# Kernel tuning notes

Hardware: AMD Instinct MI355X
Metric: run time of the kernel (lower is better)

The kernel has to match this reference:

```python
import jax, jax.numpy as jnp
import numpy as np

BATCH, T, H, N = 16, 4096, 512, 512  # batch, seq_len, d_model, d_hidden
R_MAX, R_MIN, MAX_PHASE = 1.0, 0.0, 6.28


def setup_inputs() -> dict:
    key = jax.random.key(0)
    ks = jax.random.split(key, 8)
    u_k = jax.random.normal(ks[0], (BATCH, T, H), jnp.float32)
    x0_real = jnp.zeros((BATCH, N), jnp.float32)
    x0_imag = jnp.zeros((BATCH, N), jnp.float32)
    # LRU eigenvalue parameterization (Orvieto et al. 2023)
    u1 = jax.random.uniform(ks[1], (N,), jnp.float32)
    u2 = jax.random.uniform(ks[2], (N,), jnp.float32)
    nu_log = jnp.log(-0.5 * jnp.log(u1 * (R_MAX**2 - R_MIN**2) + R_MIN**2))
    theta_log = jnp.log(MAX_PHASE * u2)
    B_re = jax.random.normal(ks[3], (N, H), jnp.float32) / np.sqrt(2.0 * H)
    B_im = jax.random.normal(ks[4], (N, H), jnp.float32) / np.sqrt(2.0 * H)
    C_re = jax.random.normal(ks[5], (H, N), jnp.float32) / np.sqrt(N)
    C_im = jax.random.normal(ks[6], (H, N), jnp.float32) / np.sqrt(N)
    D = jax.random.normal(ks[7], (H,), jnp.float32)
    return dict(x0_real=x0_real, x0_imag=x0_imag, u_k=u_k, nu_log=nu_log,
                theta_log=theta_log, B_re=B_re, B_im=B_im, C_re=C_re,
                C_im=C_im, D=D)


def reference(x0_real, x0_imag, u_k, nu_log, theta_log, B_re, B_im, C_re, C_im, D):
    # diagonal complex eigenvalues lambda in the unit disk
    lam = jnp.exp(-jnp.exp(nu_log) + 1j * jnp.exp(theta_log))          # [N] complex64
    gamma = jnp.sqrt(1.0 - jnp.abs(lam) ** 2).astype(jnp.float32)       # [N]
    Bmat = (B_re + 1j * B_im) * gamma[:, None]                          # [N,H]
    # input projection: Bu[b,t,n] = sum_h Bmat[n,h] * u[b,t,h]
    Bu = jnp.einsum('bth,nh->btn', u_k.astype(jnp.complex64), Bmat)     # [B,T,N]
    # fold initial state into first step: x_1 = lam*x_0 + Bu_1
    x0 = x0_real + 1j * x0_imag                                         # [B,N]
    Bu = Bu.at[:, 0].add(lam[None, :] * x0)
    a = jnp.broadcast_to(lam, Bu.shape)                                 # [B,T,N]

    def combine(e1, e2):
        a1, b1 = e1
        a2, b2 = e2
        return a1 * a2, a2 * b1 + b2

    # parallel associative scan of x_k = lam*x_{k-1} + Bu_k
    _, xs = jax.lax.associative_scan(combine, (a, Bu), axis=1)          # [B,T,N]
    C = C_re + 1j * C_im                                                # [H,N]
    outs = jnp.einsum('btn,hn->bth', xs, C).real + D * u_k              # [B,T,H]
    return xs[:, -1], outs
```

## Files before the change

### kernel.cpp

```cpp
#include <hip/hip_runtime.h>

#define BATCH 16
#define TSEQ  4096
#define HDIM  512
#define NDIM  512
#define NCHUNK 64
#define LCHUNK 64

using f32x4  = __attribute__((ext_vector_type(4))) float;
using bf16x8 = __attribute__((ext_vector_type(8))) short;

typedef const __attribute__((address_space(1))) void GV;
typedef __attribute__((address_space(3))) void LV;

__device__ __forceinline__ void gload16(const void* g, void* l) {
  __builtin_amdgcn_global_load_lds((GV*)g, (LV*)l, 16, 0, 0);
}
__device__ __forceinline__ unsigned short f2bf(float f) {
  unsigned u = __float_as_uint(f);
  return (unsigned short)((u + 0x7fffu + ((u >> 16) & 1u)) >> 16);
}
__device__ __forceinline__ float bf2f(unsigned short s) {
  return __uint_as_float(((unsigned)s) << 16);
}

__global__ void prep_params(const float* __restrict__ nu_log,
                            const float* __restrict__ theta_log,
                            float* lam_re, float* lam_im, float* gam,
                            float* lamL_re, float* lamL_im) {
  int n = threadIdx.x;
  float en = expf(nu_log[n]);
  float th = expf(theta_log[n]);
  float r  = expf(-en);
  lam_re[n] = r * cosf(th);
  lam_im[n] = r * sinf(th);
  float r2 = expf(-2.f * en);
  gam[n] = sqrtf(fmaxf(1.f - r2, 0.f));
  float rL  = expf(-(float)LCHUNK * en);
  float thL = (float)LCHUNK * th;
  lamL_re[n] = rL * cosf(thL);
  lamL_im[n] = rL * sinf(thL);
}

__global__ void prep_bcat(const float* __restrict__ B_re, const float* __restrict__ B_im,
                          const float* __restrict__ gam, unsigned short* __restrict__ Bcat) {
  int idx = blockIdx.x * 256 + threadIdx.x;
  int h   = idx & (HDIM - 1);
  int row = idx >> 9;
  int n   = row >> 1;
  float g = gam[n];
  float v = (row & 1) ? B_im[n * HDIM + h] : B_re[n * HDIM + h];
  Bcat[idx] = f2bf(g * v);
}

__global__ void prep_ccat(const float* __restrict__ C_re, const float* __restrict__ C_im,
                          unsigned short* __restrict__ Ccat) {
  int idx = blockIdx.x * 256 + threadIdx.x;
  int col = idx & (2 * NDIM - 1);
  int h   = idx >> 10;
  int n   = col >> 1;
  float v = (col & 1) ? -C_im[h * NDIM + n] : C_re[h * NDIM + n];
  Ccat[idx] = f2bf(v);
}

__global__ void conv_u(const float4* __restrict__ u, ushort4* __restrict__ ub, int n4) {
  int idx = blockIdx.x * 256 + threadIdx.x;
  if (idx >= n4) return;
  float4 v = u[idx];
  ushort4 o;
  o.x = f2bf(v.x); o.y = f2bf(v.y); o.z = f2bf(v.z); o.w = f2bf(v.w);
  ub[idx] = o;
}

template <int K, bool OUTBF>
__global__ __launch_bounds__(256)
void gemm97(const unsigned short* __restrict__ A,
            const unsigned short* __restrict__ Bm,
            void* __restrict__ Co, int Ncol, int Nd,
            const unsigned short* __restrict__ ub,
            const float* __restrict__ Dv) {
  __shared__ char lds[65536];
  const int tid  = threadIdx.x;
  const int wave = tid >> 6, lane = tid & 63;
  const int wr = (wave >> 1) * 64, wc = (wave & 1) * 64;

  int nwg = gridDim.x;
  int bid = blockIdx.x;
  int wg  = (bid & 7) * (nwg >> 3) + (bid >> 3);
  int bn = wg % Ncol, bm = wg / Ncol;
  const long rowBase = (long)bm * 128;
  const long colBase = (long)bn * 128;

  const int colE = 8 * ((tid & 7) ^ ((tid >> 3) & 7));
  const unsigned short* srcA[4];
  const unsigned short* srcB[4];
#pragma unroll
  for (int r = 0; r < 4; r++) {
    srcA[r] = A  + (rowBase + r * 32 + (tid >> 3)) * (long)K + colE;
    srcB[r] = Bm + (colBase + r * 32 + (tid >> 3)) * (long)K + colE;
  }

  f32x4 acc[4][4];
#pragma unroll
  for (int i = 0; i < 4; i++)
#pragma unroll
    for (int j = 0; j < 4; j++) acc[i][j] = (f32x4){0.f, 0.f, 0.f, 0.f};

  const int rsub = lane & 15;
  const int sx   = (lane & 7) << 4;
  const int ke   = (lane >> 4) << 4;

  for (int kt = 0; kt < K; kt += 64) {
    __syncthreads();
#pragma unroll
    for (int r = 0; r < 4; r++) {
      gload16(srcA[r] + kt, &lds[r * 4096 + tid * 16]);
      gload16(srcB[r] + kt, &lds[32768 + r * 4096 + tid * 16]);
    }
    __syncthreads();
#pragma unroll
    for (int kk = 0; kk < 64; kk += 32) {
      bf16x8 af[4], bf[4];
#pragma unroll
      for (int i = 0; i < 4; i++) {
        int off = (((wr + i * 16 + rsub) << 7) + kk * 2 + ke) ^ sx;
        af[i] = *(const bf16x8*)&lds[off];
      }
#pragma unroll
      for (int j = 0; j < 4; j++) {
        int off = 32768 + ((((wc + j * 16 + rsub) << 7) + kk * 2 + ke) ^ sx);
        bf[j] = *(const bf16x8*)&lds[off];
      }
#pragma unroll
      for (int i = 0; i < 4; i++)
#pragma unroll
        for (int j = 0; j < 4; j++)
          acc[i][j] = __builtin_amdgcn_mfma_f32_16x16x32_bf16(af[i], bf[j], acc[i][j], 0, 0, 0);
    }
  }

  const int cc = lane & 15, r4 = (lane >> 4) * 4;
#pragma unroll
  for (int i = 0; i < 4; i++) {
#pragma unroll
    for (int j = 0; j < 4; j++) {
      long col = colBase + wc + j * 16 + cc;
#pragma unroll
      for (int r = 0; r < 4; r++) {
        long row = rowBase + wr + i * 16 + r4 + r;
        if (OUTBF) {
          ((unsigned short*)Co)[row * (long)Nd + col] = f2bf(acc[i][j][r]);
        } else {
          float d = Dv[col];
          ((float*)Co)[row * (long)Nd + col] =
              acc[i][j][r] + d * bf2f(ub[row * (long)Nd + col]);
        }
      }
    }
  }
}

__global__ void scan_carry(const unsigned* __restrict__ Bu,
                           const float* __restrict__ lam_re, const float* __restrict__ lam_im,
                           float2* __restrict__ V) {
  int idx  = blockIdx.x * 256 + threadIdx.x;
  int n    = idx & (NDIM - 1);
  int c    = (idx >> 9) & (NCHUNK - 1);
  int bloc = idx >> 15;
  float lr = lam_re[n], li = lam_im[n];
  float xr = 0.f, xi = 0.f;
  long base = ((long)bloc * TSEQ + c * LCHUNK) * NDIM + n;
#pragma unroll 4
  for (int j = 0; j < LCHUNK; j++) {
    unsigned pv = Bu[base + (long)j * NDIM];
    float br = bf2f((unsigned short)(pv & 0xffff));
    float bi = bf2f((unsigned short)(pv >> 16));
    float nr = lr * xr - li * xi + br;
    float ni = lr * xi + li * xr + bi;
    xr = nr; xi = ni;
  }
  V[idx] = make_float2(xr, xi);
}

__global__ void scan_combine(const float2* __restrict__ V,
                             const float* __restrict__ lamL_re, const float* __restrict__ lamL_im,
                             const float* __restrict__ x0r, const float* __restrict__ x0i,
                             int b0, float2* __restrict__ In) {
  int idx  = blockIdx.x * 256 + threadIdx.x;
  int n    = idx & (NDIM - 1);
  int bloc = idx >> 9;
  int b    = b0 + bloc;
  float lr = lamL_re[n], li = lamL_im[n];
  float sr = x0r[b * NDIM + n], si = x0i[b * NDIM + n];
  long base = (long)bloc * NCHUNK * NDIM + n;
  for (int c = 0; c < NCHUNK; c++) {
    In[base + c * NDIM] = make_float2(sr, si);
    float2 v = V[base + c * NDIM];
    float nr = lr * sr - li * si + v.x;
    float ni = lr * si + li * sr + v.y;
    sr = nr; si = ni;
  }
}

__global__ void scan_apply(const unsigned* __restrict__ Bu, const float2* __restrict__ In,
                           const float* __restrict__ lam_re, const float* __restrict__ lam_im,
                           unsigned int* __restrict__ xsb, float* __restrict__ fs,
                           int b0, int fs_mode) {
  int idx  = blockIdx.x * 256 + threadIdx.x;
  int n    = idx & (NDIM - 1);
  int c    = (idx >> 9) & (NCHUNK - 1);
  int bloc = idx >> 15;
  float lr = lam_re[n], li = lam_im[n];
  float2 s = In[idx];
  float xr = s.x, xi = s.y;
  long base = ((long)bloc * TSEQ + c * LCHUNK) * NDIM + n;
#pragma unroll 4
  for (int j = 0; j < LCHUNK; j++) {
    unsigned pv = Bu[base + (long)j * NDIM];
    float br = bf2f((unsigned short)(pv & 0xffff));
    float bi = bf2f((unsigned short)(pv >> 16));
    float nr = lr * xr - li * xi + br;
    float ni = lr * xi + li * xr + bi;
    xr = nr; xi = ni;
    xsb[base + (long)j * NDIM] = (unsigned)f2bf(xr) | ((unsigned)f2bf(xi) << 16);
  }
  if (c == NCHUNK - 1 && fs_mode >= 0) {
    int b = b0 + bloc;
    if (fs_mode == 1) {
      fs[(size_t)(b * NDIM + n) * 2]     = xr;
      fs[(size_t)(b * NDIM + n) * 2 + 1] = xi;
    } else {
      fs[(size_t)(b * NDIM + n)] = xr;
    }
  }
}

extern "C" void kernel_launch(void* const* d_in, const int* in_sizes, int n_in,
                              void* d_out, int out_size, void* d_ws, size_t ws_size,
                              hipStream_t stream) {
  const float* x0r       = (const float*)d_in[0];
  const float* x0i       = (const float*)d_in[1];
  const float* u         = (const float*)d_in[2];
  const float* nu_log    = (const float*)d_in[3];
  const float* theta_log = (const float*)d_in[4];
  const float* B_re      = (const float*)d_in[5];
  const float* B_im      = (const float*)d_in[6];
  const float* C_re      = (const float*)d_in[7];
  const float* C_im      = (const float*)d_in[8];
  const float* Dv        = (const float*)d_in[9];

  char* ws = (char*)d_ws;
  size_t off = 0;
  auto alloc = [&](size_t bytes) {
    char* p = ws + off;
    off = (off + bytes + 255) & ~(size_t)255;
    return p;
  };

  float* lam_re  = (float*)alloc(NDIM * 4);
  float* lam_im  = (float*)alloc(NDIM * 4);
  float* gam     = (float*)alloc(NDIM * 4);
  float* lamL_re = (float*)alloc(NDIM * 4);
  float* lamL_im = (float*)alloc(NDIM * 4);
  unsigned short* Bcat = (unsigned short*)alloc((size_t)2 * NDIM * HDIM * 2);
  unsigned short* Ccat = (unsigned short*)alloc((size_t)HDIM * 2 * NDIM * 2);

  const size_t per_batch =
      (size_t)TSEQ * HDIM * 2 +
      (size_t)TSEQ * NDIM * 4 +
      (size_t)TSEQ * NDIM * 4 +
      (size_t)2 * NCHUNK * NDIM * 8 +
      4096;
  int G = 16;
  while (G > 1 && off + (size_t)G * per_batch > ws_size) G >>= 1;

  ushort4*      ub  = (ushort4*)alloc((size_t)G * TSEQ * HDIM * 2);
  unsigned*     Bu  = (unsigned*)alloc((size_t)G * TSEQ * NDIM * 4);
  unsigned int* xsb = (unsigned int*)alloc((size_t)G * TSEQ * NDIM * 4);
  float2*       V   = (float2*)alloc((size_t)G * NCHUNK * NDIM * 8);
  float2*       In  = (float2*)alloc((size_t)G * NCHUNK * NDIM * 8);

  const long outs_elems = (long)BATCH * TSEQ * HDIM;
  long out0 = (long)out_size - outs_elems;
  int fs_mode;
  if (out0 >= 16384)     fs_mode = 1;
  else if (out0 >= 8192) fs_mode = 0;
  else { out0 = 0;       fs_mode = -1; }

  float* fs   = (float*)d_out;
  float* outs = (float*)d_out + out0;

  prep_params<<<1, NDIM, 0, stream>>>(nu_log, theta_log, lam_re, lam_im, gam, lamL_re, lamL_im);
  prep_bcat<<<(2 * NDIM * HDIM) / 256, 256, 0, stream>>>(B_re, B_im, gam, Bcat);
  prep_ccat<<<(HDIM * 2 * NDIM) / 256, 256, 0, stream>>>(C_re, C_im, Ccat);

  for (int b0 = 0; b0 < BATCH; b0 += G) {
    const float* ug = u + (size_t)b0 * TSEQ * HDIM;
    int Mloc = G * TSEQ;
    int n4 = Mloc * HDIM / 4;
    conv_u<<<(n4 + 255) / 256, 256, 0, stream>>>((const float4*)ug, ub, n4);

    int nwg1 = (Mloc / 128) * 8;
    gemm97<512, true><<<nwg1, 256, 0, stream>>>(
        (const unsigned short*)ub, Bcat, Bu, 8, 2 * NDIM, nullptr, nullptr);

    scan_carry<<<(G * NCHUNK * NDIM) / 256, 256, 0, stream>>>(Bu, lam_re, lam_im, V);
    scan_combine<<<(G * NDIM) / 256, 256, 0, stream>>>(
        V, lamL_re, lamL_im, x0r, x0i, b0, In);
    scan_apply<<<(G * NCHUNK * NDIM) / 256, 256, 0, stream>>>(
        Bu, In, lam_re, lam_im, xsb, fs, b0, fs_mode);

    int nwg2 = (Mloc / 128) * 4;
    gemm97<1024, false><<<nwg2, 256, 0, stream>>>(
        (const unsigned short*)xsb, Ccat, outs + (size_t)b0 * TSEQ * HDIM,
        4, HDIM, (const unsigned short*)ub, Dv);
  }
}
```

Measured before the change: 348.1 us.

## Double-buffer LDS tiles in GEMM to overlap global loads with MFMA

```diff
diff --git a/kernel.cpp b/kernel.cpp
--- a/kernel.cpp
+++ b/kernel.cpp
@@ -73,7 +73,7 @@
 }
 
 template <int K, bool OUTBF>
-__global__ __launch_bounds__(256)
+__global__ __launch_bounds__(256, 2)
 void gemm97(const unsigned short* __restrict__ A,
             const unsigned short* __restrict__ Bm,
             void* __restrict__ Co, int Ncol, int Nd,
@@ -110,25 +110,42 @@
   const int sx   = (lane & 7) << 4;
   const int ke   = (lane >> 4) << 4;
 
-  for (int kt = 0; kt < K; kt += 64) {
-    __syncthreads();
+  auto STAGE = [&](int p, int kt) {
+    char* base = &lds[p * 32768];
 #pragma unroll
     for (int r = 0; r < 4; r++) {
-      gload16(srcA[r] + kt, &lds[r * 4096 + tid * 16]);
-      gload16(srcB[r] + kt, &lds[32768 + r * 4096 + tid * 16]);
-    }
-    __syncthreads();
-#pragma unroll
-    for (int kk = 0; kk < 64; kk += 32) {
+      gload16(srcA[r] + kt, base + r * 4096 + tid * 16);
+      gload16(srcB[r] + kt, base + 16384 + r * 4096 + tid * 16);
+    }
+  };
+
+#define BAR() asm volatile("s_barrier" ::: "memory")
+
+  const int NT = K / 64;
+  STAGE(0, 0);
+
+#pragma unroll 2
+  for (int t = 0; t < NT; t++) {
+    const int p = t & 1;
+    if (t + 1 < NT) {
+      STAGE(p ^ 1, (t + 1) * 64);
+      asm volatile("s_waitcnt vmcnt(8)" ::: "memory");
+    } else {
+      asm volatile("s_waitcnt vmcnt(0)" ::: "memory");
+    }
+    BAR();
+    const int po = p * 32768;
+#pragma unroll
+    for (int kk2 = 0; kk2 < 2; kk2++) {
       bf16x8 af[4], bf[4];
 #pragma unroll
       for (int i = 0; i < 4; i++) {
-        int off = (((wr + i * 16 + rsub) << 7) + kk * 2 + ke) ^ sx;
+        int off = po + ((((wr + i * 16 + rsub) << 7) + kk2 * 64 + ke) ^ sx);
         af[i] = *(const bf16x8*)&lds[off];
       }
 #pragma unroll
       for (int j = 0; j < 4; j++) {
-        int off = 32768 + ((((wc + j * 16 + rsub) << 7) + kk * 2 + ke) ^ sx);
+        int off = po + 16384 + ((((wc + j * 16 + rsub) << 7) + kk2 * 64 + ke) ^ sx);
         bf[j] = *(const bf16x8*)&lds[off];
       }
 #pragma unroll
@@ -137,7 +154,9 @@
         for (int j = 0; j < 4; j++)
           acc[i][j] = __builtin_amdgcn_mfma_f32_16x16x32_bf16(af[i], bf[j], acc[i][j], 0, 0, 0);
     }
-  }
+    BAR();
+  }
+#undef BAR
 
   const int cc = lane & 15, r4 = (lane >> 4) * 4;
 #pragma unroll
```

After: 319.6 us. 1.09x faster.
